# Performance work log

Hardware: AMD Instinct MI355X
Metric: run time of the kernel (lower is better)

Reference implementation:

```python
import jax, jax.numpy as jnp
import numpy as np

S, N, C_M, C_Z, C, H = 256, 384, 64, 128, 32, 8


def _layer_norm(x, w, b, eps=1e-5):
    mu = x.mean(axis=-1, keepdims=True)
    var = x.var(axis=-1, keepdims=True)
    return (x - mu) / jnp.sqrt(var + eps) * w + b


def setup_inputs() -> dict:
    key = jax.random.key(0)
    ks = jax.random.split(key, 8)
    m = jax.random.normal(ks[0], (S, N, C_M), dtype=jnp.float32)
    z = jax.random.normal(ks[1], (N, N, C_Z), dtype=jnp.float32)
    single_mask = jax.random.bernoulli(ks[2], 0.9, (N,))
    scale = 0.02
    return {
        "m": m,
        "z": z,
        "single_mask": single_mask,
        "ln_m_w": jnp.ones((C_M,), jnp.float32),
        "ln_m_b": jnp.zeros((C_M,), jnp.float32),
        "ln_z_w": jnp.ones((C_Z,), jnp.float32),
        "ln_z_b": jnp.zeros((C_Z,), jnp.float32),
        "w_v": jax.random.normal(ks[3], (C_M, H * C), jnp.float32) * scale,
        "w_b": jax.random.normal(ks[4], (C_Z, H), jnp.float32) * scale,
        "w_g": jax.random.normal(ks[5], (C_M, H * C), jnp.float32) * scale,
        "w_out": jax.random.normal(ks[6], (H * C, C_M), jnp.float32) * scale,
    }


def reference(m, z, single_mask, ln_m_w, ln_m_b, ln_z_w, ln_z_b, w_v, w_b, w_g, w_out):
    # m: [s, i, c_m], z: [i, j, c_z], single_mask: [j] bool
    m_ln = _layer_norm(m, ln_m_w, ln_m_b)
    v = (m_ln @ w_v).reshape(S, N, H, C)          # [s, j, h, c]
    b = _layer_norm(z, ln_z_w, ln_z_b) @ w_b      # [i, j, h]
    g = jax.nn.sigmoid(m_ln @ w_g)                # [s, i, h*c]
    # mask broadcast over j axis: [..., None, :, None]
    b = b + jnp.where(single_mask[None, :, None], 0.0, -1e9)
    w = jax.nn.softmax(b, axis=-2)                # softmax over j
    o = jnp.einsum('ijh,sjhc->sihc', w, v)        # [s, i, h, c]
    o = g * o.reshape(S, N, H * C)
    return o @ w_out                               # [s, i, c_m]
```

## Files before the change

kernel.cpp:

```cpp
#include <hip/hip_runtime.h>
#include <math.h>


#define SS 256
#define NN 384
#define CM 64
#define CZ 128
#define HH 8
#define HC 256
#define NV 25165824

typedef __attribute__((ext_vector_type(8))) short short8v;
typedef __attribute__((ext_vector_type(8))) unsigned short ushort8v;
typedef __attribute__((ext_vector_type(4))) unsigned short ushort4v;
typedef __attribute__((ext_vector_type(4))) float f32x4;

static __device__ __forceinline__ float bf2f(unsigned short u) {
    union { unsigned int i; float f; } x; x.i = ((unsigned int)u) << 16; return x.f;
}
static __device__ __forceinline__ unsigned short f2bf(float f) {
    union { float f; unsigned int i; } x; x.f = f;
    unsigned int r = x.i + 0x7FFFu + ((x.i >> 16) & 1u);
    return (unsigned short)(r >> 16);
}
static __device__ __forceinline__ void gload_lds16(const void* g, void* l) {
    __builtin_amdgcn_global_load_lds((const __attribute__((address_space(1))) void*)g,
                                     (__attribute__((address_space(3))) void*)l, 16, 0, 0);
}

__global__ __launch_bounds__(256) void k_prep(
    const unsigned int* __restrict__ mu, const float* __restrict__ lnzw,
    const float* __restrict__ lnzb, const float* __restrict__ w_b,
    const float* __restrict__ w_v, const float* __restrict__ w_g,
    float* __restrict__ mterm, unsigned short* __restrict__ w2bf,
    float* __restrict__ consts, unsigned short* __restrict__ BTg)
{
    const int b = blockIdx.x, tid = threadIdx.x;
    if (b == 0) {
        __shared__ int byteLayout;
        if (tid == 0) byteLayout = 0;
        __syncthreads();
        if (tid < 96) {
            unsigned int u = mu[tid];
            if (u != 0u && u != 1u && u != 0x3F800000u) atomicOr(&byteLayout, 1);
        }
        __syncthreads();
        for (int j = tid; j < 384; j += 256) {
            int val;
            if (byteLayout) val = ((const unsigned char*)mu)[j];
            else            val = (mu[j] != 0u);
            mterm[j] = val ? 0.0f : -1e9f;
        }
    } else if (b == 1) {
        __shared__ float pA[128][8], pB[128][8];
        const int c = tid & 127;
        if (tid < 128) {
            float lw = lnzw[c], lb = lnzb[c];
            float4 wb0 = *(const float4*)&w_b[c * 8];
            float4 wb1 = *(const float4*)&w_b[c * 8 + 4];
            float wv[8] = {wb0.x, wb0.y, wb0.z, wb0.w, wb1.x, wb1.y, wb1.z, wb1.w};
            #pragma unroll
            for (int h = 0; h < 8; h++) {
                w2bf[h * CZ + c]       = f2bf(lw * wv[h]);
                w2bf[(8 + h) * CZ + c] = 0;
                pA[c][h] = lw * wv[h];
                pB[c][h] = lb * wv[h];
            }
        }
        __syncthreads();
        if (tid < 8) {
            float A = 0.f, B = 0.f;
            for (int q = 0; q < 128; q++) { A += pA[q][tid]; B += pB[q][tid]; }
            consts[tid] = A; consts[16 + tid] = B;
            consts[8 + tid] = 0.f; consts[24 + tid] = 0.f;
        }
    } else {
        const int col = (b - 2) * 4 + (tid >> 6);
        const int k   = tid & 63;
        float w = (col < 256) ? w_v[k * 256 + col] : w_g[k * 256 + (col - 256)];
        BTg[col * 64 + (k ^ ((col & 7) << 3))] = f2bf(w);
    }
}

__global__ __launch_bounds__(512) void k1b23(
    const unsigned short* __restrict__ BTg, const float* __restrict__ m,
    const float* __restrict__ lnw, const float* __restrict__ lnb,
    unsigned short* __restrict__ vT, unsigned short* __restrict__ gout,
    const float* __restrict__ z, const unsigned short* __restrict__ w2bf,
    const float* __restrict__ consts, const float* __restrict__ mterm,
    unsigned short* __restrict__ wbl)
{
    __shared__ unsigned short SMEM[36864];
    const int tid = threadIdx.x, wid = tid >> 6, lane = tid & 63;
    const int rl = lane & 15, kc = lane >> 4;

    if (blockIdx.x < 384) {
        unsigned short* Llog = SMEM;
        const int i = blockIdx.x;

        short8v bf[4];
        #pragma unroll
        for (int ks = 0; ks < 4; ks++)
            bf[ks] = *(const short8v*)&w2bf[rl * CZ + ks * 32 + kc * 8];
        const float Ah = consts[rl], Bh = consts[16 + rl];

        #pragma unroll
        for (int ch = 0; ch < 3; ch++) {
            const int jb = wid * 48 + ch * 16;
            const float* zr = z + ((size_t)i * NN + jb + rl) * CZ + kc * 8;

            float s1 = 0.f, s2 = 0.f;
            short8v af[4];
            #pragma unroll
            for (int ks = 0; ks < 4; ks++) {
                float4 z0 = *(const float4*)(zr + ks * 32);
                float4 z1 = *(const float4*)(zr + ks * 32 + 4);
                float zz[8] = {z0.x, z0.y, z0.z, z0.w, z1.x, z1.y, z1.z, z1.w};
                short8v a;
                #pragma unroll
                for (int q = 0; q < 8; q++) {
                    s1 += zz[q];
                    s2 += zz[q] * zz[q];
                    a[q] = (short)f2bf(zz[q]);
                }
                af[ks] = a;
            }
            s1 += __shfl_xor(s1, 16); s2 += __shfl_xor(s2, 16);
            s1 += __shfl_xor(s1, 32); s2 += __shfl_xor(s2, 32);

            f32x4 acc = {};
            #pragma unroll
            for (int ks = 0; ks < 4; ks++)
                acc = __builtin_amdgcn_mfma_f32_16x16x32_bf16(af[ks], bf[ks], acc, 0, 0, 0);

            unsigned short pv[4];
            #pragma unroll
            for (int reg = 0; reg < 4; reg++) {
                int r = 4 * kc + reg;
                float S1 = __shfl(s1, r);
                float S2 = __shfl(s2, r);
                float mu   = S1 * (1.0f / CZ);
                float var  = S2 * (1.0f / CZ) - mu * mu;
                float rstd = rsqrtf(var + 1e-5f);
                float b = rstd * acc[reg] - rstd * mu * Ah + Bh + mterm[jb + r];
                pv[reg] = f2bf(b);
            }
            if (rl < 8) {
                #pragma unroll
                for (int reg = 0; reg < 4; reg++)
                    Llog[(jb + 4 * kc + reg) * 10 + rl] = pv[reg];
            }
        }
        __syncthreads();

        unsigned short* p = wbl + ((size_t)wid * NN + i) * NN;
        float x[6];
        float mx = -1e30f;
        #pragma unroll
        for (int e = 0; e < 6; e++) { x[e] = bf2f(Llog[(lane + e * 64) * 10 + wid]); mx = fmaxf(mx, x[e]); }
        #pragma unroll
        for (int off = 32; off; off >>= 1) mx = fmaxf(mx, __shfl_xor(mx, off));
        float sum = 0.f;
        #pragma unroll
        for (int e = 0; e < 6; e++) { x[e] = expf(x[e] - mx); sum += x[e]; }
        #pragma unroll
        for (int off = 32; off; off >>= 1) sum += __shfl_xor(sum, off);
        float inv = 1.0f / sum;
        #pragma unroll
        for (int e = 0; e < 6; e++) p[lane + e * 64] = f2bf(x[e] * inv);
        return;
    }

    unsigned short* Wl = SMEM;
    unsigned short* Al = SMEM + 32768;
    const int fam = wid >> 2, wq = wid & 3;
    const int rowBase = (blockIdx.x - 384) * 64;
    const int s = rowBase / NN, j0 = rowBase - s * NN;

    const float lw = lnw[lane], lb = lnb[lane];
    float mx8[8];
    #pragma unroll
    for (int rr = 0; rr < 8; rr++)
        mx8[rr] = m[(size_t)(rowBase + wid * 8 + rr) * CM + lane];
    __builtin_amdgcn_sched_barrier(0);

    #pragma unroll
    for (int it = 0; it < 8; it++) {
        int eoff = wid * 4096 + it * 512;
        gload_lds16(BTg + eoff + lane * 8, (void*)((char*)Wl + eoff * 2));
    }
    __builtin_amdgcn_sched_barrier(0);

    #pragma unroll
    for (int rr = 0; rr < 8; rr++) {
        int row = wid * 8 + rr;
        float x = mx8[rr];
        float s1 = x, s2 = x * x;
        #pragma unroll
        for (int off = 32; off; off >>= 1) {
            s1 += __shfl_xor(s1, off);
            s2 += __shfl_xor(s2, off);
        }
        float mu  = s1 * (1.0f / CM);
        float var = s2 * (1.0f / CM) - mu * mu;
        float y = (x - mu) * rsqrtf(var + 1e-5f) * lw + lb;
        Al[row * 64 + (lane ^ ((row & 7) << 3))] = f2bf(y);
    }

    asm volatile("s_waitcnt lgkmcnt(0)" ::: "memory");
    __builtin_amdgcn_s_barrier();
    __builtin_amdgcn_sched_barrier(0);
    asm volatile("s_waitcnt vmcnt(0)" ::: "memory");
    __builtin_amdgcn_sched_barrier(0);

    short8v al[2][4];
    #pragma unroll
    for (int ks = 0; ks < 2; ks++)
        #pragma unroll
        for (int q = 0; q < 4; q++) {
            int row = q * 16 + rl;
            al[ks][q] = *(const short8v*)&Al[(row * 64 + ks * 32 + kc * 8) ^ ((row & 7) << 3)];
        }

    unsigned short* WP = Wl + wid * 4096;
    unsigned short* VS = WP;

    f32x4 acc[4][4] = {};
    if (fam == 0) {
        #pragma unroll
        for (int ks = 0; ks < 2; ks++) {
            short8v wf[4];
            #pragma unroll
            for (int q = 0; q < 4; q++) {
                int cl = q * 16 + rl;
                wf[q] = *(const short8v*)&WP[(cl * 64 + ks * 32 + kc * 8) ^ ((cl & 7) << 3)];
            }
            #pragma unroll
            for (int mi = 0; mi < 4; mi++)
                #pragma unroll
                for (int nf = 0; nf < 4; nf++)
                    acc[mi][nf] = __builtin_amdgcn_mfma_f32_16x16x32_bf16(al[ks][mi], wf[nf], acc[mi][nf], 0, 0, 0);
        }
        #pragma unroll
        for (int mi = 0; mi < 4; mi++) {
            const int jb = mi * 16 + kc * 4;
            #pragma unroll
            for (int nf = 0; nf < 4; nf++) {
                int hcl = nf * 16 + rl;
                ushort4v o4;
                #pragma unroll
                for (int r = 0; r < 4; r++) o4[r] = f2bf(acc[mi][nf][r]);
                *(ushort4v*)&VS[(hcl * 64 + jb) ^ ((hcl & 7) << 3)] = o4;
            }
        }
        #pragma unroll
        for (int p = 0; p < 8; p++) {
            int hcl = p * 8 + (lane >> 3);
            int j8  = (lane & 7) * 8;
            ushort8v val = *(const ushort8v*)&VS[(hcl * 64 + j8) ^ ((hcl & 7) << 3)];
            int hc = wq * 64 + hcl;
            size_t vrow = (size_t)((hc >> 5) * 8192 + s * 32 + (hc & 31));
            *(ushort8v*)&vT[vrow * NN + j0 + j8] = val;
        }
    } else {
        #pragma unroll
        for (int ks = 0; ks < 2; ks++) {
            short8v wf[4];
            #pragma unroll
            for (int q = 0; q < 4; q++) {
                int cl = q * 16 + rl;
                wf[q] = *(const short8v*)&WP[(cl * 64 + ks * 32 + kc * 8) ^ ((cl & 7) << 3)];
            }
            #pragma unroll
            for (int mi = 0; mi < 4; mi++)
                #pragma unroll
                for (int nf = 0; nf < 4; nf++)
                    acc[mi][nf] = __builtin_amdgcn_mfma_f32_16x16x32_bf16(wf[mi], al[ks][nf], acc[mi][nf], 0, 0, 0);
        }
        #pragma unroll
        for (int mi = 0; mi < 4; mi++) {
            const int hcb = mi * 16 + kc * 4;
            #pragma unroll
            for (int nf = 0; nf < 4; nf++) {
                int rowl = nf * 16 + rl;
                ushort4v o4;
                #pragma unroll
                for (int r = 0; r < 4; r++)
                    o4[r] = f2bf(1.0f / (1.0f + __expf(-acc[mi][nf][r])));
                *(ushort4v*)&VS[(rowl * 64 + hcb) ^ ((rowl & 7) << 3)] = o4;
            }
        }
        #pragma unroll
        for (int p = 0; p < 8; p++) {
            int rowl = p * 8 + (lane >> 3);
            int hc8  = (lane & 7) * 8;
            ushort8v val = *(const ushort8v*)&VS[(rowl * 64 + hc8) ^ ((rowl & 7) << 3)];
            *(ushort8v*)&gout[(size_t)(rowBase + rowl) * HC + wq * 64 + hc8] = val;
        }
    }
}

__global__ __launch_bounds__(256) void k4_mfma(
    const unsigned short* __restrict__ wbf, const unsigned short* __restrict__ vT,
    unsigned short* __restrict__ ob)
{
    __shared__ unsigned short Al[128 * 32];
    __shared__ unsigned short Bl[128 * 32];
    const int tid  = threadIdx.x;
    const int wid  = tid >> 6, lane = tid & 63;
    const int wm   = wid >> 1, wn = wid & 1;
    const int h    = blockIdx.z;
    const int i0   = blockIdx.y * 128;
    const int n0   = blockIdx.x * 128;
    const unsigned short* Ag = wbf + (size_t)h * NN * NN;
    const unsigned short* Bg = vT  + (size_t)h * 8192 * NN;

    f32x4 acc[4][4] = {};

    const int lrow = lane >> 2, lchunk = lane & 3;
    for (int k0 = 0; k0 < NN; k0 += 32) {
        #pragma unroll
        for (int q = 0; q < 2; q++) {
            int issue = wid * 2 + q;
            int r = issue * 16 + lrow;
            gload_lds16(Ag + (size_t)(i0 + r) * NN + k0 + lchunk * 8,
                        (void*)((char*)Al + issue * 1024));
            gload_lds16(Bg + (size_t)(n0 + r) * NN + k0 + lchunk * 8,
                        (void*)((char*)Bl + issue * 1024));
        }
        __syncthreads();

        short8v a[4], b[4];
        #pragma unroll
        for (int mi = 0; mi < 4; mi++)
            a[mi] = *(const short8v*)&Al[(wm * 64 + mi * 16 + (lane & 15)) * 32 + (lane >> 4) * 8];
        #pragma unroll
        for (int ni = 0; ni < 4; ni++)
            b[ni] = *(const short8v*)&Bl[(wn * 64 + ni * 16 + (lane & 15)) * 32 + (lane >> 4) * 8];
        #pragma unroll
        for (int mi = 0; mi < 4; mi++)
            #pragma unroll
            for (int ni = 0; ni < 4; ni++)
                acc[mi][ni] = __builtin_amdgcn_mfma_f32_16x16x32_bf16(b[ni], a[mi], acc[mi][ni], 0, 0, 0);
        __syncthreads();
    }

    #pragma unroll
    for (int mi = 0; mi < 4; mi++) {
        const int i = i0 + wm * 64 + mi * 16 + (lane & 15);
        #pragma unroll
        for (int ni = 0; ni < 4; ni++) {
            const int sc0 = n0 + wn * 64 + ni * 16 + ((lane >> 4) << 2);
            const int s = sc0 >> 5, c0 = sc0 & 31;
            ushort4v o4;
            #pragma unroll
            for (int r = 0; r < 4; r++) o4[r] = f2bf(acc[mi][ni][r]);
            *(ushort4v*)&ob[((size_t)s * NN + i) * HC + (h << 5) + c0] = o4;
        }
    }
}

__global__ __launch_bounds__(256) void k5_mfma(
    const unsigned short* __restrict__ ob, const unsigned short* __restrict__ g,
    const float* __restrict__ w_out, float* __restrict__ out)
{
    __shared__ unsigned short WT[64 * 256];
    const int tid = threadIdx.x, wid = tid >> 6, lane = tid & 63;
    #pragma unroll
    for (int e = 0; e < 16; e++) {
        int fidx = (tid + e * 256) * 4;
        float4 w4 = *(const float4*)&w_out[fidx];
        int k = fidx >> 6, c0 = fidx & 63;
        float wv[4] = {w4.x, w4.y, w4.z, w4.w};
        #pragma unroll
        for (int q = 0; q < 4; q++) {
            int c = c0 + q;
            WT[(((c << 8) + k)) ^ ((c & 7) << 3)] = f2bf(wv[q]);
        }
    }
    __syncthreads();

    const size_t rowbase = (size_t)blockIdx.x * 64 + wid * 16;
    const int arow = lane & 15, achunk = lane >> 4;
    const unsigned short* op = ob + (rowbase + arow) * HC + achunk * 8;
    const unsigned short* gp = g  + (rowbase + arow) * HC + achunk * 8;

    f32x4 acc[4] = {};
    #pragma unroll
    for (int ks = 0; ks < 8; ks++) {
        ushort8v o8 = *(const ushort8v*)(op + ks * 32);
        ushort8v g8 = *(const ushort8v*)(gp + ks * 32);
        short8v a;
        #pragma unroll
        for (int q = 0; q < 8; q++)
            a[q] = (short)f2bf(bf2f(o8[q]) * bf2f(g8[q]));
        #pragma unroll
        for (int nf = 0; nf < 4; nf++) {
            const int c = nf * 16 + arow;
            short8v b = *(const short8v*)&WT[(((c << 8) + ks * 32 + achunk * 8)) ^ ((c & 7) << 3)];
            acc[nf] = __builtin_amdgcn_mfma_f32_16x16x32_bf16(a, b, acc[nf], 0, 0, 0);
        }
    }
    #pragma unroll
    for (int nf = 0; nf < 4; nf++)
        #pragma unroll
        for (int r = 0; r < 4; r++)
            out[(rowbase + achunk * 4 + r) * CM + nf * 16 + arow] = acc[nf][r];
}

extern "C" void kernel_launch(void* const* d_in, const int* in_sizes, int n_in,
                              void* d_out, int out_size, void* d_ws, size_t ws_size,
                              hipStream_t stream)
{
    const float* m      = (const float*)d_in[0];
    const float* z      = (const float*)d_in[1];
    const unsigned int* mask_raw = (const unsigned int*)d_in[2];
    const float* ln_m_w = (const float*)d_in[3];
    const float* ln_m_b = (const float*)d_in[4];
    const float* ln_z_w = (const float*)d_in[5];
    const float* ln_z_b = (const float*)d_in[6];
    const float* w_v    = (const float*)d_in[7];
    const float* w_b    = (const float*)d_in[8];
    const float* w_g    = (const float*)d_in[9];
    const float* w_out  = (const float*)d_in[10];
    float* out = (float*)d_out;

    float* mterm = (float*)d_ws;
    unsigned short* wbl = (unsigned short*)(mterm + 384);
    unsigned short* vT  = wbl + 1179648;
    unsigned short* g   = vT + NV;
    unsigned short* ob  = g + NV;
    unsigned short* BTg = ob + NV;
    unsigned short* w2bf = BTg + 32768;
    float* consts = (float*)(w2bf + 2048);

    k_prep<<<130, 256, 0, stream>>>(mask_raw, ln_z_w, ln_z_b, w_b, w_v, w_g,
                                    mterm, w2bf, consts, BTg);
    k1b23<<<1920, 512, 0, stream>>>(BTg, m, ln_m_w, ln_m_b, vT, g,
                                    z, w2bf, consts, mterm, wbl);
    k4_mfma<<<dim3(64, 3, 8), 256, 0, stream>>>(wbl, vT, ob);
    k5_mfma<<<1536, 256, 0, stream>>>(ob, g, w_out, out);
}
```

Measured before the change: 123.9 us.

## Move m layer norm into prep kernel and async-load bf16 result into LDS

LayerNorm of m is now computed in extra blocks of the prep kernel and written as swizzled bf16 into the ob workspace buffer, which is later overwritten. The projection kernel then loads these pre-normalized tiles directly into LDS with global_load_lds instead of loading fp32 m, reducing with shuffles and writing LDS itself. This removes a serial load-reduce-store phase and a barrier from the GEMM prologue, at the cost of an extra write and read of a bf16 copy of m. It also adds a larger prep launch.

```diff
diff --git a/kernel.cpp b/kernel.cpp
--- a/kernel.cpp
+++ b/kernel.cpp
@@ -28,14 +28,37 @@
                                      (__attribute__((address_space(3))) void*)l, 16, 0, 0);
 }
 
-__global__ __launch_bounds__(256) void k_prep(
+__global__ __launch_bounds__(256) void k_prep1(
     const unsigned int* __restrict__ mu, const float* __restrict__ lnzw,
     const float* __restrict__ lnzb, const float* __restrict__ w_b,
     const float* __restrict__ w_v, const float* __restrict__ w_g,
+    const float* __restrict__ m, const float* __restrict__ lnw, const float* __restrict__ lnb,
     float* __restrict__ mterm, unsigned short* __restrict__ w2bf,
-    float* __restrict__ consts, unsigned short* __restrict__ BTg)
+    float* __restrict__ consts, unsigned short* __restrict__ BTg,
+    unsigned short* __restrict__ mln)
 {
     const int b = blockIdx.x, tid = threadIdx.x;
+    if (b >= 130) {
+        const int wid = tid >> 6, lane = tid & 63;
+        const int rowBase = (b - 130) * 64 + wid * 16;
+        const float lw = lnw[lane], lb2 = lnb[lane];
+        #pragma unroll 4
+        for (int rr = 0; rr < 16; rr++) {
+            int row = rowBase + rr;
+            float x = m[(size_t)row * CM + lane];
+            float s1 = x, s2 = x * x;
+            #pragma unroll
+            for (int off = 32; off; off >>= 1) {
+                s1 += __shfl_xor(s1, off);
+                s2 += __shfl_xor(s2, off);
+            }
+            float mu2  = s1 * (1.0f / CM);
+            float var = s2 * (1.0f / CM) - mu2 * mu2;
+            float y = (x - mu2) * rsqrtf(var + 1e-5f) * lw + lb2;
+            mln[(size_t)row * CM + (lane ^ ((row & 7) << 3))] = f2bf(y);
+        }
+        return;
+    }
     if (b == 0) {
         __shared__ int byteLayout;
         if (tid == 0) byteLayout = 0;
@@ -55,7 +78,7 @@
         __shared__ float pA[128][8], pB[128][8];
         const int c = tid & 127;
         if (tid < 128) {
-            float lw = lnzw[c], lb = lnzb[c];
+            float lw = lnzw[c], lb2 = lnzb[c];
             float4 wb0 = *(const float4*)&w_b[c * 8];
             float4 wb1 = *(const float4*)&w_b[c * 8 + 4];
             float wv[8] = {wb0.x, wb0.y, wb0.z, wb0.w, wb1.x, wb1.y, wb1.z, wb1.w};
@@ -64,7 +87,7 @@
                 w2bf[h * CZ + c]       = f2bf(lw * wv[h]);
                 w2bf[(8 + h) * CZ + c] = 0;
                 pA[c][h] = lw * wv[h];
-                pB[c][h] = lb * wv[h];
+                pB[c][h] = lb2 * wv[h];
             }
         }
         __syncthreads();
@@ -83,8 +106,7 @@
 }
 
 __global__ __launch_bounds__(512) void k1b23(
-    const unsigned short* __restrict__ BTg, const float* __restrict__ m,
-    const float* __restrict__ lnw, const float* __restrict__ lnb,
+    const unsigned short* __restrict__ BTg, const unsigned short* __restrict__ mln,
     unsigned short* __restrict__ vT, unsigned short* __restrict__ gout,
     const float* __restrict__ z, const unsigned short* __restrict__ w2bf,
     const float* __restrict__ consts, const float* __restrict__ mterm,
@@ -177,39 +199,16 @@
     const int rowBase = (blockIdx.x - 384) * 64;
     const int s = rowBase / NN, j0 = rowBase - s * NN;
 
-    const float lw = lnw[lane], lb = lnb[lane];
-    float mx8[8];
-    #pragma unroll
-    for (int rr = 0; rr < 8; rr++)
-        mx8[rr] = m[(size_t)(rowBase + wid * 8 + rr) * CM + lane];
-    __builtin_amdgcn_sched_barrier(0);
-
     #pragma unroll
     for (int it = 0; it < 8; it++) {
         int eoff = wid * 4096 + it * 512;
         gload_lds16(BTg + eoff + lane * 8, (void*)((char*)Wl + eoff * 2));
     }
-    __builtin_amdgcn_sched_barrier(0);
-
-    #pragma unroll
-    for (int rr = 0; rr < 8; rr++) {
-        int row = wid * 8 + rr;
-        float x = mx8[rr];
-        float s1 = x, s2 = x * x;
-        #pragma unroll
-        for (int off = 32; off; off >>= 1) {
-            s1 += __shfl_xor(s1, off);
-            s2 += __shfl_xor(s2, off);
-        }
-        float mu  = s1 * (1.0f / CM);
-        float var = s2 * (1.0f / CM) - mu * mu;
-        float y = (x - mu) * rsqrtf(var + 1e-5f) * lw + lb;
-        Al[row * 64 + (lane ^ ((row & 7) << 3))] = f2bf(y);
-    }
-
-    asm volatile("s_waitcnt lgkmcnt(0)" ::: "memory");
-    __builtin_amdgcn_s_barrier();
-    __builtin_amdgcn_sched_barrier(0);
+    #pragma unroll
+    for (int it = 0; it < 8; it++) {
+        int eoff = it * 512;
+        gload_lds16(mln + (size_t)rowBase * CM + eoff + lane * 8, (void*)((char*)Al + eoff * 2));
+    }
     asm volatile("s_waitcnt vmcnt(0)" ::: "memory");
     __builtin_amdgcn_sched_barrier(0);
 
@@ -433,11 +432,12 @@
     unsigned short* BTg = ob + NV;
     unsigned short* w2bf = BTg + 32768;
     float* consts = (float*)(w2bf + 2048);
-
-    k_prep<<<130, 256, 0, stream>>>(mask_raw, ln_z_w, ln_z_b, w_b, w_v, w_g,
-                                    mterm, w2bf, consts, BTg);
-    k1b23<<<1920, 512, 0, stream>>>(BTg, m, ln_m_w, ln_m_b, vT, g,
-                                    z, w2bf, consts, mterm, wbl);
+    unsigned short* mln = ob;
+
+    k_prep1<<<1666, 256, 0, stream>>>(mask_raw, ln_z_w, ln_z_b, w_b, w_v, w_g,
+                                      m, ln_m_w, ln_m_b,
+                                      mterm, w2bf, consts, BTg, mln);
+    k1b23<<<1920, 512, 0, stream>>>(BTg, mln, vT, g, z, w2bf, consts, mterm, wbl);
     k4_mfma<<<dim3(64, 3, 8), 256, 0, stream>>>(wbl, vT, ob);
     k5_mfma<<<1536, 256, 0, stream>>>(ob, g, w_out, out);
 }
```

Result: no change. 123.3 us (-0.5%).
